# Kernel optimization log

Hardware: AMD Instinct MI355X
Metric: run time of the kernel (lower is better)

Reference implementation:

```python
import jax, jax.numpy as jnp
import numpy as np

B, T, E, H = 4, 4096, 512, 64

def setup_inputs() -> dict:
    key = jax.random.key(0)
    k1, k2, k3, k4 = jax.random.split(key, 4)
    x = jax.random.normal(k1, (B, T, E), dtype=jnp.float32)
    # nn.Linear(E, H, bias=False) weight has shape [H, E]; y = x @ W.T
    Wq = jax.random.normal(k2, (H, E), dtype=jnp.float32) * (E ** -0.5)
    Wk = jax.random.normal(k3, (H, E), dtype=jnp.float32) * (E ** -0.5)
    Wv = jax.random.normal(k4, (H, E), dtype=jnp.float32) * (E ** -0.5)
    return {"x": x, "Wq": Wq, "Wk": Wk, "Wv": Wv}

def reference(x, Wq, Wk, Wv):
    # projections: [B, T, H]
    q = jnp.einsum('bte,he->bth', x, Wq)
    k = jnp.einsum('bte,he->bth', x, Wk)
    v = jnp.einsum('bte,he->bth', x, Wv)
    scale = 1.0 / jnp.sqrt(jnp.float32(q.shape[-1]))
    scores = jnp.einsum('bth,bsh->bts', q, k) * scale  # [B, T, T]
    t = scores.shape[-1]
    causal = jnp.tril(jnp.ones((t, t), dtype=bool))
    scores = jnp.where(causal, scores, -jnp.inf)
    probs = jax.nn.softmax(scores, axis=-1)
    # dropout p=0.0 (eval) -> identity
    return jnp.einsum('bts,bsh->bth', probs, v)
```

## Files before the change

### kernel.cpp

```cpp
#include <hip/hip_runtime.h>
#include <hip/hip_bf16.h>

#define Bn 4
#define Tn 4096
#define En 512
#define Hn 64
#define NEGINF -3e38f
#define QSCALE 0.1803368801f

typedef __attribute__((ext_vector_type(8))) __bf16 bf16x8;
typedef __attribute__((ext_vector_type(4))) __bf16 bf16x4;
typedef __attribute__((ext_vector_type(4))) float f32x4;

#define MFMA16(a, b, c) __builtin_amdgcn_mfma_f32_16x16x32_bf16(a, b, c, 0, 0, 0)

__device__ __forceinline__ float bf2f(unsigned short u) {
    union { unsigned u; float f; } v; v.u = ((unsigned)u) << 16;
    return v.f;
}
__device__ __forceinline__ unsigned cvtpk(float a, float b) {
    unsigned d;
    asm("v_cvt_pk_bf16_f32 %0, %1, %2" : "=v"(d) : "v"(a), "v"(b));
    return d;
}
__device__ __forceinline__ unsigned short f2bf(float f) {
    union { float f; unsigned u; } v; v.f = f;
    unsigned r = v.u + 0x7fffu + ((v.u >> 16) & 1u);
    return (unsigned short)(r >> 16);
}
__device__ __forceinline__ float exp2fast(float x) {
    float r;
    asm("v_exp_f32 %0, %1" : "=v"(r) : "v"(x));
    return r;
}
__device__ __forceinline__ void gl16(const void* g, void* l) {
    __builtin_amdgcn_global_load_lds(
        (const __attribute__((address_space(1))) unsigned int*)g,
        (__attribute__((address_space(3))) unsigned int*)l, 16, 0, 0);
}

__launch_bounds__(256, 2)
__global__ void proj(const float* __restrict__ x, const float* __restrict__ Wq,
                     const float* __restrict__ Wk, const float* __restrict__ Wv,
                     unsigned short* __restrict__ q16, unsigned short* __restrict__ k16,
                     unsigned short* __restrict__ vt16) {
    __shared__ __align__(16) unsigned char plds[2][28672];
    const int tid = threadIdx.x;
    const int w = tid >> 6, lane = tid & 63, r = lane & 15, g = lane >> 4;
    const int row0 = blockIdx.x * 32;
    const int rsel = (w & 1) * 16, csel = (w >> 1) * 96;

    const int srow = tid >> 3, skc = (tid & 7) * 8;
    const int sby = (tid & 7) * 16;

    f32x4 acc[6];
#pragma unroll
    for (int i = 0; i < 6; ++i) acc[i] = (f32x4){0.f, 0.f, 0.f, 0.f};

    {
        const float4* xp = (const float4*)&x[(row0 + srow) * En + skc];
        float4 f0 = xp[0], f1 = xp[1];
        union { bf16x8 v; unsigned u32[4]; } t;
        t.u32[0] = cvtpk(f0.x, f0.y); t.u32[1] = cvtpk(f0.z, f0.w);
        t.u32[2] = cvtpk(f1.x, f1.y); t.u32[3] = cvtpk(f1.z, f1.w);
        *(bf16x8*)&plds[0][srow * 128 + (sby ^ ((srow & 7) << 4))] = t.v;
#pragma unroll
        for (int c2 = 0; c2 < 6; ++c2) {
            const float* Ws = (c2 < 2) ? Wq : ((c2 < 4) ? Wk : Wv);
            int wr = (c2 & 1) * 32 + srow;
            const float4* wp = (const float4*)&Ws[wr * En + skc];
            float4 w0 = wp[0], w1 = wp[1];
            union { bf16x8 v; unsigned u32[4]; } tw;
            tw.u32[0] = cvtpk(w0.x, w0.y); tw.u32[1] = cvtpk(w0.z, w0.w);
            tw.u32[2] = cvtpk(w1.x, w1.y); tw.u32[3] = cvtpk(w1.z, w1.w);
            int wrow = c2 * 32 + srow;
            *(bf16x8*)&plds[0][4096 + wrow * 128 + (sby ^ ((wrow & 7) << 4))] = tw.v;
        }
    }
    __syncthreads();

    for (int s = 0; s < 8; ++s) {
        const int pp = s & 1;
        const bool more = (s < 7);
        float4 nf0, nf1;
        float4 nw0[6], nw1[6];
        if (more) {
            int k1 = (s + 1) * 64;
            const float4* xp = (const float4*)&x[(row0 + srow) * En + k1 + skc];
            nf0 = xp[0]; nf1 = xp[1];
#pragma unroll
            for (int c2 = 0; c2 < 6; ++c2) {
                const float* Ws = (c2 < 2) ? Wq : ((c2 < 4) ? Wk : Wv);
                int wr = (c2 & 1) * 32 + srow;
                const float4* wp = (const float4*)&Ws[wr * En + k1 + skc];
                nw0[c2] = wp[0]; nw1[c2] = wp[1];
            }
        }
        {
            const unsigned char* A = &plds[pp][0];
            const unsigned char* W = &plds[pp][4096];
            int arow = rsel + r, asw = (arow & 7) << 4;
            bf16x8 a0 = *(const bf16x8*)&A[arow * 128 + ((g * 16) ^ asw)];
            bf16x8 a1 = *(const bf16x8*)&A[arow * 128 + ((64 + g * 16) ^ asw)];
#pragma unroll
            for (int ct = 0; ct < 6; ++ct) {
                int wrow = csel + ct * 16 + r, wsw = (wrow & 7) << 4;
                bf16x8 b0 = *(const bf16x8*)&W[wrow * 128 + ((g * 16) ^ wsw)];
                bf16x8 b1 = *(const bf16x8*)&W[wrow * 128 + ((64 + g * 16) ^ wsw)];
                acc[ct] = MFMA16(a0, b0, acc[ct]);
                acc[ct] = MFMA16(a1, b1, acc[ct]);
            }
        }
        if (more) {
            unsigned char* D = &plds[pp ^ 1][0];
            union { bf16x8 v; unsigned u32[4]; } t;
            t.u32[0] = cvtpk(nf0.x, nf0.y); t.u32[1] = cvtpk(nf0.z, nf0.w);
            t.u32[2] = cvtpk(nf1.x, nf1.y); t.u32[3] = cvtpk(nf1.z, nf1.w);
            *(bf16x8*)&D[srow * 128 + (sby ^ ((srow & 7) << 4))] = t.v;
#pragma unroll
            for (int c2 = 0; c2 < 6; ++c2) {
                union { bf16x8 v; unsigned u32[4]; } tw;
                tw.u32[0] = cvtpk(nw0[c2].x, nw0[c2].y); tw.u32[1] = cvtpk(nw0[c2].z, nw0[c2].w);
                tw.u32[2] = cvtpk(nw1[c2].x, nw1[c2].y); tw.u32[3] = cvtpk(nw1[c2].z, nw1[c2].w);
                int wrow = c2 * 32 + srow;
                *(bf16x8*)&D[4096 + wrow * 128 + (sby ^ ((wrow & 7) << 4))] = tw.v;
            }
        }
        __syncthreads();
    }
#pragma unroll
    for (int ct = 0; ct < 6; ++ct) {
        int n = csel + ct * 16 + r;
#pragma unroll
        for (int reg = 0; reg < 4; ++reg) {
            int gr = row0 + rsel + g * 4 + reg;
            if (n < 64) {
                q16[gr * 64 + n] = f2bf(acc[ct][reg] * QSCALE);
            } else if (n < 128) {
                k16[gr * 64 + (n - 64)] = f2bf(acc[ct][reg]);
            } else {
                int h = n - 128; int bb = gr >> 12; int t = gr & 4095;
                vt16[((bb * 64 + h) << 12) + t] = f2bf(acc[ct][reg]);
            }
        }
    }
}

__launch_bounds__(256, 4)
__global__ void attnp(const unsigned short* __restrict__ q16, const unsigned short* __restrict__ k16,
                      const unsigned short* __restrict__ vt16,
                      unsigned short* __restrict__ po, float* __restrict__ lp) {
    __shared__ __align__(16) unsigned char lds[2][16384];

    const int tid = threadIdx.x;
    const int w = tid >> 6, lane = tid & 63, r = lane & 15, g = lane >> 4;
    const int bid = blockIdx.x;
    const int k_ = bid >> 8, idx = bid & 255;
    const int s5 = idx >> 3, b = (idx >> 1) & 3, q1 = idx & 1;
    const int jt = (k_ & 1) ? s5 : 63 - s5;
    const int quarter = ((k_ >> 1) << 1) | q1;
    const size_t kbase = (size_t)b * Tn;
    const int q0 = jt * 64;
    const int nt = jt + 1;
    const int t0 = (quarter * nt) >> 2;
    const int tEnd = ((quarter + 1) * nt) >> 2;
    const int wq0 = q0 + w * 16;

    const unsigned short* Kb = k16 + kbase * 64;
    const unsigned short* Vb = vt16 + ((size_t)(b * 64) << 12);

    const int srl = lane >> 3, scb = (lane & 7) * 16;

    bf16x8 bq0, bq1;
    {
        const unsigned short* qp = &q16[(kbase + wq0 + r) * 64 + g * 8];
        bq0 = *(const bf16x8*)qp;
        bq1 = *(const bf16x8*)(qp + 32);
    }

    f32x4 o[4];
#pragma unroll
    for (int i = 0; i < 4; ++i) o[i] = (f32x4){0.f, 0.f, 0.f, 0.f};
    float l_ = 0.f;

    if (tEnd > t0) {
        int kv0 = t0 * 64;
        unsigned char* D = &lds[t0 & 1][0];
#pragma unroll
        for (int i = 0; i < 4; ++i) {
            int cc = w * 4 + i;
            if (cc < 8) {
                int row = cc * 8 + srl, sw = (row & 7) << 4;
                gl16((const char*)Kb + (size_t)(kv0 + row) * 128 + (scb ^ sw), D + cc * 1024);
            } else {
                int h = (cc - 8) * 8 + srl, sw = (h & 7) << 4;
                gl16((const char*)Vb + (size_t)h * 8192 + (size_t)kv0 * 2 + (scb ^ sw), D + cc * 1024);
            }
        }
    }

    for (int it = t0; it < tEnd; ++it) {
        const int pp = it & 1;
        asm volatile("s_waitcnt vmcnt(0)" ::: "memory");
        __builtin_amdgcn_s_barrier();
        __builtin_amdgcn_sched_barrier(0);
        if (it + 1 < tEnd) {
            int nkv = (it + 1) * 64;
            unsigned char* D = &lds[pp ^ 1][0];
#pragma unroll
            for (int i = 0; i < 4; ++i) {
                int cc = w * 4 + i;
                if (cc < 8) {
                    int row = cc * 8 + srl, sw = (row & 7) << 4;
                    gl16((const char*)Kb + (size_t)(nkv + row) * 128 + (scb ^ sw), D + cc * 1024);
                } else {
                    int h = (cc - 8) * 8 + srl, sw = (h & 7) << 4;
                    gl16((const char*)Vb + (size_t)h * 8192 + (size_t)nkv * 2 + (scb ^ sw), D + cc * 1024);
                }
            }
        }
        const int kv0 = it * 64;
        if (kv0 <= wq0 + 15) {
            const unsigned char* K = &lds[pp][0];
            const unsigned char* V = &lds[pp][8192];
            f32x4 s4[4];
            __builtin_amdgcn_s_setprio(1);
#pragma unroll
            for (int ct = 0; ct < 4; ++ct) {
                int row = ct * 16 + r;
                int base = row * 128, sw = (row & 7) << 4;
                bf16x8 ak0 = *(const bf16x8*)&K[base + ((g * 16) ^ sw)];
                bf16x8 ak1 = *(const bf16x8*)&K[base + ((64 + g * 16) ^ sw)];
                f32x4 t = (f32x4){0.f, 0.f, 0.f, 0.f};
                t = MFMA16(ak0, bq0, t);
                t = MFMA16(ak1, bq1, t);
                s4[ct] = t;
            }
            __builtin_amdgcn_s_setprio(0);
            if (kv0 + 63 > wq0) {
                int qq = wq0 + r;
#pragma unroll
                for (int ct = 0; ct < 4; ++ct)
#pragma unroll
                    for (int reg = 0; reg < 4; ++reg) {
                        int kv = kv0 + ct * 16 + g * 4 + reg;
                        if (kv > qq) s4[ct][reg] = NEGINF;
                    }
            }
#pragma unroll
            for (int ct = 0; ct < 4; ++ct)
#pragma unroll
                for (int reg = 0; reg < 4; ++reg)
                    s4[ct][reg] = exp2fast(s4[ct][reg]);
            l_ += ((s4[0][0] + s4[0][1]) + (s4[0][2] + s4[0][3])) +
                  ((s4[1][0] + s4[1][1]) + (s4[1][2] + s4[1][3])) +
                  ((s4[2][0] + s4[2][1]) + (s4[2][2] + s4[2][3])) +
                  ((s4[3][0] + s4[3][1]) + (s4[3][2] + s4[3][3]));
            union { bf16x8 v; unsigned u32[4]; } pk[2];
#pragma unroll
            for (int kf = 0; kf < 2; ++kf) {
                pk[kf].u32[0] = cvtpk(s4[kf * 2][0], s4[kf * 2][1]);
                pk[kf].u32[1] = cvtpk(s4[kf * 2][2], s4[kf * 2][3]);
                pk[kf].u32[2] = cvtpk(s4[kf * 2 + 1][0], s4[kf * 2 + 1][1]);
                pk[kf].u32[3] = cvtpk(s4[kf * 2 + 1][2], s4[kf * 2 + 1][3]);
            }
            __builtin_amdgcn_s_setprio(1);
#pragma unroll
            for (int cth = 0; cth < 4; ++cth) {
                int h = cth * 16 + r;
                int vb = h * 128, sw2 = (h & 7) << 4;
#pragma unroll
                for (int kf = 0; kf < 2; ++kf) {
                    int off = kf * 64 + g * 8;
                    union { bf16x8 v; bf16x4 h4[2]; } vv;
                    vv.h4[0] = *(const bf16x4*)&V[vb + (off ^ sw2)];
                    vv.h4[1] = *(const bf16x4*)&V[vb + ((off + 32) ^ sw2)];
                    o[cth] = MFMA16(pk[kf].v, vv.v, o[cth]);
                }
            }
            __builtin_amdgcn_s_setprio(0);
        }
    }

    const size_t qb = (size_t)quarter * 16384 + b * 4096;
#pragma unroll
    for (int cth = 0; cth < 4; ++cth)
#pragma unroll
        for (int reg = 0; reg < 4; ++reg)
            po[(qb + wq0 + g * 4 + reg) * 64 + cth * 16 + r] = f2bf(o[cth][reg]);
    lp[(qb + wq0 + r) * 4 + g] = l_;
}

__global__ void merge(const unsigned short* __restrict__ po, const float* __restrict__ lp,
                      float* __restrict__ out) {
    int t = blockIdx.x * 256 + threadIdx.x;
    int q = t >> 3, c8 = (t & 7) * 8;
    float L = 0.f;
#pragma unroll
    for (int c = 0; c < 4; ++c)
#pragma unroll
        for (int gg = 0; gg < 4; ++gg)
            L += lp[((size_t)c * 16384 + q) * 4 + gg];
    float inv = 1.0f / L;
    float acc[8] = {0.f, 0.f, 0.f, 0.f, 0.f, 0.f, 0.f, 0.f};
#pragma unroll
    for (int c = 0; c < 4; ++c) {
        union { uint4 v; unsigned short u[8]; } ld;
        ld.v = *(const uint4*)&po[((size_t)c * 16384 + q) * 64 + c8];
#pragma unroll
        for (int j = 0; j < 8; ++j) acc[j] += bf2f(ld.u[j]);
    }
    float4* op = (float4*)&out[(size_t)q * 64 + c8];
    op[0] = (float4){acc[0] * inv, acc[1] * inv, acc[2] * inv, acc[3] * inv};
    op[1] = (float4){acc[4] * inv, acc[5] * inv, acc[6] * inv, acc[7] * inv};
}

extern "C" void kernel_launch(void* const* d_in, const int* in_sizes, int n_in,
                              void* d_out, int out_size, void* d_ws, size_t ws_size,
                              hipStream_t stream) {
    const float* x  = (const float*)d_in[0];
    const float* Wq = (const float*)d_in[1];
    const float* Wk = (const float*)d_in[2];
    const float* Wv = (const float*)d_in[3];
    float* out = (float*)d_out;
    char* ws = (char*)d_ws;

    unsigned short* q16 = (unsigned short*)ws;
    unsigned short* k16 = (unsigned short*)(ws + 2097152);
    unsigned short* v16 = (unsigned short*)(ws + 4194304);
    unsigned short* po  = (unsigned short*)(ws + 6291456);
    float*          lp  = (float*)(ws + 14680064);

    hipLaunchKernelGGL(proj, dim3(512), dim3(256), 0, stream, x, Wq, Wk, Wv, q16, k16, v16);
    hipLaunchKernelGGL(attnp, dim3(1024), dim3(256), 0, stream, q16, k16, v16, po, lp);
    hipLaunchKernelGGL(merge, dim3(512), dim3(256), 0, stream, po, lp, out);
}
```

Baseline: 44.38 us.

## Double query tile per block to reuse K/V tiles across two query fragments

Each attention block now covers 128 query rows (32 per wave, two 16-row fragments) instead of 64, so every K/V tile loaded into LDS and every K/V fragment read from LDS feeds twice as many MFMAs. To keep the grid at 1024 blocks, the KV range is split into 8 pieces instead of 4, and the merge kernel now sums 8 partial outputs. This lowers LDS and global traffic per FLOP, at the cost of more registers per thread (which may hurt occupancy under launch bounds 4), doubled partial-output storage, and more merge work.

```diff
diff --git a/kernel.cpp b/kernel.cpp
--- a/kernel.cpp
+++ b/kernel.cpp
@@ -155,33 +155,36 @@
     const int tid = threadIdx.x;
     const int w = tid >> 6, lane = tid & 63, r = lane & 15, g = lane >> 4;
     const int bid = blockIdx.x;
-    const int k_ = bid >> 8, idx = bid & 255;
+    const int page = bid >> 8, idx = bid & 255;
     const int s5 = idx >> 3, b = (idx >> 1) & 3, q1 = idx & 1;
-    const int jt = (k_ & 1) ? s5 : 63 - s5;
-    const int quarter = ((k_ >> 1) << 1) | q1;
+    const int jt = (page & 1) ? s5 : 31 - s5;
+    const int piece = ((page & 1) << 2) | ((page >> 1) << 1) | q1;
     const size_t kbase = (size_t)b * Tn;
-    const int q0 = jt * 64;
-    const int nt = jt + 1;
-    const int t0 = (quarter * nt) >> 2;
-    const int tEnd = ((quarter + 1) * nt) >> 2;
-    const int wq0 = q0 + w * 16;
+    const int q0 = jt * 128;
+    const int nt = 2 * (jt + 1);
+    const int t0 = (piece * nt) >> 3;
+    const int tEnd = ((piece + 1) * nt) >> 3;
+    const int wq0 = q0 + w * 32;
 
     const unsigned short* Kb = k16 + kbase * 64;
     const unsigned short* Vb = vt16 + ((size_t)(b * 64) << 12);
 
     const int srl = lane >> 3, scb = (lane & 7) * 16;
 
-    bf16x8 bq0, bq1;
-    {
-        const unsigned short* qp = &q16[(kbase + wq0 + r) * 64 + g * 8];
-        bq0 = *(const bf16x8*)qp;
-        bq1 = *(const bf16x8*)(qp + 32);
-    }
-
-    f32x4 o[4];
-#pragma unroll
-    for (int i = 0; i < 4; ++i) o[i] = (f32x4){0.f, 0.f, 0.f, 0.f};
-    float l_ = 0.f;
+    bf16x8 bq[2][2];
+#pragma unroll
+    for (int qf = 0; qf < 2; ++qf) {
+        const unsigned short* qp = &q16[(kbase + wq0 + qf * 16 + r) * 64 + g * 8];
+        bq[qf][0] = *(const bf16x8*)qp;
+        bq[qf][1] = *(const bf16x8*)(qp + 32);
+    }
+
+    f32x4 o[2][4];
+#pragma unroll
+    for (int qf = 0; qf < 2; ++qf)
+#pragma unroll
+        for (int i = 0; i < 4; ++i) o[qf][i] = (f32x4){0.f, 0.f, 0.f, 0.f};
+    float l_[2] = {0.f, 0.f};
 
     if (tEnd > t0) {
         int kv0 = t0 * 64;
@@ -220,10 +223,10 @@
             }
         }
         const int kv0 = it * 64;
-        if (kv0 <= wq0 + 15) {
+        if (kv0 <= wq0 + 31) {
             const unsigned char* K = &lds[pp][0];
             const unsigned char* V = &lds[pp][8192];
-            f32x4 s4[4];
+            f32x4 s4[2][4];
             __builtin_amdgcn_s_setprio(1);
 #pragma unroll
             for (int ct = 0; ct < 4; ++ct) {
@@ -231,38 +234,47 @@
                 int base = row * 128, sw = (row & 7) << 4;
                 bf16x8 ak0 = *(const bf16x8*)&K[base + ((g * 16) ^ sw)];
                 bf16x8 ak1 = *(const bf16x8*)&K[base + ((64 + g * 16) ^ sw)];
-                f32x4 t = (f32x4){0.f, 0.f, 0.f, 0.f};
-                t = MFMA16(ak0, bq0, t);
-                t = MFMA16(ak1, bq1, t);
-                s4[ct] = t;
+#pragma unroll
+                for (int qf = 0; qf < 2; ++qf) {
+                    f32x4 t = (f32x4){0.f, 0.f, 0.f, 0.f};
+                    t = MFMA16(ak0, bq[qf][0], t);
+                    t = MFMA16(ak1, bq[qf][1], t);
+                    s4[qf][ct] = t;
+                }
             }
             __builtin_amdgcn_s_setprio(0);
             if (kv0 + 63 > wq0) {
-                int qq = wq0 + r;
+#pragma unroll
+                for (int qf = 0; qf < 2; ++qf) {
+                    int qq = wq0 + qf * 16 + r;
+#pragma unroll
+                    for (int ct = 0; ct < 4; ++ct)
+#pragma unroll
+                        for (int reg = 0; reg < 4; ++reg) {
+                            int kv = kv0 + ct * 16 + g * 4 + reg;
+                            if (kv > qq) s4[qf][ct][reg] = NEGINF;
+                        }
+                }
+            }
+            union { bf16x8 v; unsigned u32[4]; } pk[2][2];
+#pragma unroll
+            for (int qf = 0; qf < 2; ++qf) {
 #pragma unroll
                 for (int ct = 0; ct < 4; ++ct)
 #pragma unroll
-                    for (int reg = 0; reg < 4; ++reg) {
-                        int kv = kv0 + ct * 16 + g * 4 + reg;
-                        if (kv > qq) s4[ct][reg] = NEGINF;
-                    }
-            }
-#pragma unroll
-            for (int ct = 0; ct < 4; ++ct)
-#pragma unroll
-                for (int reg = 0; reg < 4; ++reg)
-                    s4[ct][reg] = exp2fast(s4[ct][reg]);
-            l_ += ((s4[0][0] + s4[0][1]) + (s4[0][2] + s4[0][3])) +
-                  ((s4[1][0] + s4[1][1]) + (s4[1][2] + s4[1][3])) +
-                  ((s4[2][0] + s4[2][1]) + (s4[2][2] + s4[2][3])) +
-                  ((s4[3][0] + s4[3][1]) + (s4[3][2] + s4[3][3]));
-            union { bf16x8 v; unsigned u32[4]; } pk[2];
-#pragma unroll
-            for (int kf = 0; kf < 2; ++kf) {
-                pk[kf].u32[0] = cvtpk(s4[kf * 2][0], s4[kf * 2][1]);
-                pk[kf].u32[1] = cvtpk(s4[kf * 2][2], s4[kf * 2][3]);
-                pk[kf].u32[2] = cvtpk(s4[kf * 2 + 1][0], s4[kf * 2 + 1][1]);
-                pk[kf].u32[3] = cvtpk(s4[kf * 2 + 1][2], s4[kf * 2 + 1][3]);
+                    for (int reg = 0; reg < 4; ++reg)
+                        s4[qf][ct][reg] = exp2fast(s4[qf][ct][reg]);
+                l_[qf] += ((s4[qf][0][0] + s4[qf][0][1]) + (s4[qf][0][2] + s4[qf][0][3])) +
+                          ((s4[qf][1][0] + s4[qf][1][1]) + (s4[qf][1][2] + s4[qf][1][3])) +
+                          ((s4[qf][2][0] + s4[qf][2][1]) + (s4[qf][2][2] + s4[qf][2][3])) +
+                          ((s4[qf][3][0] + s4[qf][3][1]) + (s4[qf][3][2] + s4[qf][3][3]));
+#pragma unroll
+                for (int kf = 0; kf < 2; ++kf) {
+                    pk[qf][kf].u32[0] = cvtpk(s4[qf][kf * 2][0], s4[qf][kf * 2][1]);
+                    pk[qf][kf].u32[1] = cvtpk(s4[qf][kf * 2][2], s4[qf][kf * 2][3]);
+                    pk[qf][kf].u32[2] = cvtpk(s4[qf][kf * 2 + 1][0], s4[qf][kf * 2 + 1][1]);
+                    pk[qf][kf].u32[3] = cvtpk(s4[qf][kf * 2 + 1][2], s4[qf][kf * 2 + 1][3]);
+                }
             }
             __builtin_amdgcn_s_setprio(1);
 #pragma unroll
@@ -275,20 +287,24 @@
                     union { bf16x8 v; bf16x4 h4[2]; } vv;
                     vv.h4[0] = *(const bf16x4*)&V[vb + (off ^ sw2)];
                     vv.h4[1] = *(const bf16x4*)&V[vb + ((off + 32) ^ sw2)];
-                    o[cth] = MFMA16(pk[kf].v, vv.v, o[cth]);
+                    o[0][cth] = MFMA16(pk[0][kf].v, vv.v, o[0][cth]);
+                    o[1][cth] = MFMA16(pk[1][kf].v, vv.v, o[1][cth]);
                 }
             }
             __builtin_amdgcn_s_setprio(0);
         }
     }
 
-    const size_t qb = (size_t)quarter * 16384 + b * 4096;
-#pragma unroll
-    for (int cth = 0; cth < 4; ++cth)
-#pragma unroll
-        for (int reg = 0; reg < 4; ++reg)
-            po[(qb + wq0 + g * 4 + reg) * 64 + cth * 16 + r] = f2bf(o[cth][reg]);
-    lp[(qb + wq0 + r) * 4 + g] = l_;
+    const size_t qb = (size_t)piece * 16384 + b * 4096;
+#pragma unroll
+    for (int qf = 0; qf < 2; ++qf) {
+#pragma unroll
+        for (int cth = 0; cth < 4; ++cth)
+#pragma unroll
+            for (int reg = 0; reg < 4; ++reg)
+                po[(qb + wq0 + qf * 16 + g * 4 + reg) * 64 + cth * 16 + r] = f2bf(o[qf][cth][reg]);
+        lp[(qb + wq0 + qf * 16 + r) * 4 + g] = l_[qf];
+    }
 }
 
 __global__ void merge(const unsigned short* __restrict__ po, const float* __restrict__ lp,
@@ -297,14 +313,14 @@
     int q = t >> 3, c8 = (t & 7) * 8;
     float L = 0.f;
 #pragma unroll
-    for (int c = 0; c < 4; ++c)
+    for (int c = 0; c < 8; ++c)
 #pragma unroll
         for (int gg = 0; gg < 4; ++gg)
             L += lp[((size_t)c * 16384 + q) * 4 + gg];
     float inv = 1.0f / L;
     float acc[8] = {0.f, 0.f, 0.f, 0.f, 0.f, 0.f, 0.f, 0.f};
 #pragma unroll
-    for (int c = 0; c < 4; ++c) {
+    for (int c = 0; c < 8; ++c) {
         union { uint4 v; unsigned short u[8]; } ld;
         ld.v = *(const uint4*)&po[((size_t)c * 16384 + q) * 64 + c8];
 #pragma unroll
@@ -329,7 +345,7 @@
     unsigned short* k16 = (unsigned short*)(ws + 2097152);
     unsigned short* v16 = (unsigned short*)(ws + 4194304);
     unsigned short* po  = (unsigned short*)(ws + 6291456);
-    float*          lp  = (float*)(ws + 14680064);
+    float*          lp  = (float*)(ws + 23068672);
 
     hipLaunchKernelGGL(proj, dim3(512), dim3(256), 0, stream, x, Wq, Wk, Wv, q16, k16, v16);
     hipLaunchKernelGGL(attnp, dim3(1024), dim3(256), 0, stream, q16, k16, v16, po, lp);
```

Result: faster. 42.42 us (-4.4%).
